# Performance work log

Hardware: AMD Instinct MI355X
Metric: run time of the kernel (lower is better)

The kernel has to match this reference:

```python
import jax, jax.numpy as jnp
import numpy as np


def setup_inputs() -> dict:
    key = jax.random.key(0)
    k1, k2, k3 = jax.random.split(key, 3)
    n_way, n_shot, d, n_query = 5, 10, 1024, 16384
    n_support = n_way * n_shot
    train_imgs = jax.random.normal(k1, (n_support, d), dtype=jnp.float32)
    # one-hot labels: exactly n_shot examples per class (interleaved)
    cls = jnp.tile(jnp.arange(n_way), n_shot)  # [n_support]
    train_labels = jax.nn.one_hot(cls, n_way, dtype=jnp.int64)
    query_imgs = jax.random.normal(k2, (n_query, d), dtype=jnp.float32)
    query_labels = jax.random.randint(k3, (n_query,), 0, n_way)
    return {"train_imgs": train_imgs, "train_labels": train_labels,
            "query_imgs": query_imgs, "query_labels": query_labels}


def reference(train_imgs, train_labels, query_imgs, query_labels):
    # backbone = identity: imgs are already feature embeddings
    n_support, n_way = train_labels.shape
    n_shot = n_support // n_way  # static
    support = train_imgs                      # [n_support, d]
    query = query_imgs                        # [n_query, d]

    # group support features by class: [n_way, n_shot, d]
    cls = jnp.argmax(train_labels, axis=1)
    order = jnp.argsort(cls, stable=True)
    grouped = support[order].reshape(n_way, n_shot, -1)
    mats = jnp.swapaxes(grouped, 1, 2)        # [n_way, d, n_shot]

    # batched reduced SVD (torch.svd some=True -> full_matrices=False)
    U, _, _ = jnp.linalg.svd(mats, full_matrices=False)  # [n_way, d, n_shot]
    Uk = U[:, :, : n_shot - 1]                # [n_way, d, k]

    # projection of queries onto each class subspace: P = Uk Uk^T q
    coeff = jnp.einsum('wdk,qd->wkq', Uk, query)   # [n_way, k, n_query]
    proj = jnp.einsum('wdk,wkq->wqd', Uk, coeff)   # [n_way, n_query, d]
    dist = jnp.sum((query[None, :, :] - proj) ** 2, axis=-1)  # [n_way, n_query]

    logits = -dist.T                           # [n_query, n_way]
    # normalize=False in this configuration
    return jax.nn.log_softmax(logits, axis=1)
```

## Files before the change

### kernel.cpp

```cpp
#include <hip/hip_runtime.h>
#include <stdint.h>


typedef __attribute__((ext_vector_type(4))) float f32x4;
typedef __attribute__((ext_vector_type(8))) short s16x8;

#define WS_G_OFF    0
#define WS_GH_OFF   4096
#define WS_P_OFF    8192
#define WS_Z_OFF    262144

__device__ __forceinline__ unsigned short f2bf(float f) {
  unsigned int u = __float_as_uint(f);
  u += 0x7FFFu + ((u >> 16) & 1u);
  return (unsigned short)(u >> 16);
}

__device__ __forceinline__ bool labels_int64(const int* L) {
  int cnt = 0; bool oddz = true;
  #pragma unroll
  for (int t = 0; t < 20; ++t) {
    int v = L[t];
    if (t & 1) { if (v) oddz = false; }
    else       { if (v) cnt++; }
  }
  return oddz && (cnt == 2);
}

__device__ __forceinline__ int cls_of(const int* L, bool is64, int i) {
  int best = -0x7fffffff, c = 0;
  #pragma unroll
  for (int j = 0; j < 5; ++j) {
    int v = is64 ? L[i * 10 + 2 * j] : L[i * 5 + j];
    if (v > best) { best = v; c = j; }
  }
  return c;
}

__global__ __launch_bounds__(256) void dsn_prep(const float* __restrict__ support,
                                                const int* __restrict__ labels,
                                                double* __restrict__ G,
                                                unsigned short* __restrict__ P) {
  int b = blockIdx.x;
  bool is64 = labels_int64(labels);

  if (b < 69) {
    int wid  = b * 4 + (threadIdx.x >> 6);
    int lane = threadIdx.x & 63;
    if (wid >= 275) return;
    int w = wid / 55, p = wid % 55;
    int a = 0;
    while (p >= 10 - a) { p -= 10 - a; a++; }
    int bb = a + p;

    int myc = (lane < 50) ? cls_of(labels, is64, lane) : -1;
    unsigned long long mask = __ballot(lane < 50 && myc == w);

    unsigned long long m = mask;
    for (int i = 0; i < a; ++i) m &= m - 1;
    int ia = __ffsll((unsigned long long)m) - 1;
    m = mask;
    for (int i = 0; i < bb; ++i) m &= m - 1;
    int ib = __ffsll((unsigned long long)m) - 1;

    const float* A = support + ia * 1024;
    const float* B = support + ib * 1024;
    double acc = 0.0;
    #pragma unroll
    for (int i = 0; i < 16; ++i) {
      int d = lane + 64 * i;
      acc += (double)A[d] * (double)B[d];
    }
    #pragma unroll
    for (int off = 32; off > 0; off >>= 1) acc += __shfl_xor(acc, off);
    if (lane == 0) {
      G[(w * 10 + a) * 10 + bb] = acc;
      G[(w * 10 + bb) * 10 + a] = acc;
    }
  } else {
    int r = b - 69;
    int w = r >> 4, kk = r & 15;
    int t = threadIdx.x;
    unsigned short* Prow = P + r * 1024;
    if (kk >= 10) {
      #pragma unroll
      for (int j = 0; j < 4; ++j) Prow[t + 256 * j] = 0;
      return;
    }
    __shared__ int sid;
    if (t < 64) {
      int myc = (t < 50) ? cls_of(labels, is64, t) : -1;
      unsigned long long mask = __ballot(t < 50 && myc == w);
      if (t == 0) {
        unsigned long long m = mask;
        for (int z = 0; z < kk; ++z) m &= m - 1;
        sid = __ffsll(m) - 1;
      }
    }
    __syncthreads();
    const float* src = support + (size_t)sid * 1024;
    #pragma unroll
    for (int j = 0; j < 4; ++j) Prow[t + 256 * j] = f2bf(src[t + 256 * j]);
  }
}

__global__ __launch_bounds__(64) void dsn_zs(const float* __restrict__ query,
                                             const unsigned short* __restrict__ P,
                                             const double* __restrict__ G,
                                             float* __restrict__ Ghat,
                                             float* __restrict__ Z) {
  if (blockIdx.x < 5) {
    __shared__ float Gf[100], B[100];
    __shared__ float rowk[10], colk[10], vbuf[10], gvbuf[10];
    __shared__ float sbuf;
    __shared__ int   jmx;

    int w = blockIdx.x, t = threadIdx.x;
    bool act = (t < 50);
    int e0 = 2 * t, e1 = 2 * t + 1;
    int i0 = e0 / 10, j0 = e0 % 10;
    int i1 = e1 / 10, j1 = e1 % 10;
    if (!act) { e0 = 0; e1 = 1; i0 = 0; j0 = 0; i1 = 0; j1 = 1; }

    float a0 = 0.f, a1 = 0.f;
    if (act) {
      a0 = (float)G[w * 100 + e0];
      a1 = (float)G[w * 100 + e1];
      Gf[e0] = a0; Gf[e1] = a1;
    }
    __syncthreads();

    #pragma unroll 1
    for (int k = 0; k < 10; ++k) {
      if (act) {
        if (i0 == k) rowk[j0] = a0;
        if (i1 == k) rowk[j1] = a1;
        if (j0 == k) colk[i0] = a0;
        if (j1 == k) colk[i1] = a1;
      }
      __syncthreads();
      float dinv = 1.f / rowk[k];
      float r0 = rowk[j0], c0 = colk[i0];
      float r1 = rowk[j1], c1 = colk[i1];
      __syncthreads();
      if (act) {
        bool ik = (i0 == k), jk = (j0 == k);
        if (ik && jk)        a0 = -dinv;
        else if (ik || jk)   a0 = a0 * dinv;
        else                 a0 -= c0 * r0 * dinv;
        ik = (i1 == k); jk = (j1 == k);
        if (ik && jk)        a1 = -dinv;
        else if (ik || jk)   a1 = a1 * dinv;
        else                 a1 -= c1 * r1 * dinv;
      }
    }
    float ginv0 = -a0, ginv1 = -a1;

    if (act) { B[e0] = ginv0; B[e1] = ginv1; }
    __syncthreads();
    if (t == 0) {
      float m = B[0];
      #pragma unroll
      for (int k = 1; k < 10; ++k) m = fmaxf(m, B[k * 10 + k]);
      sbuf = 1.f / m;
    }
    __syncthreads();
    float rm0 = sbuf;
    if (act) { B[e0] = ginv0 * rm0; B[e1] = ginv1 * rm0; }
    __syncthreads();

    #pragma unroll 1
    for (int sq = 0; sq < 7; ++sq) {
      float s0 = 0.f, s1 = 0.f;
      if (act) {
        #pragma unroll
        for (int k = 0; k < 10; ++k) {
          s0 += B[i0 * 10 + k] * B[k * 10 + j0];
          s1 += B[i1 * 10 + k] * B[k * 10 + j1];
        }
      }
      __syncthreads();
      if (act) { B[e0] = s0; B[e1] = s1; }
      __syncthreads();
      if (t == 0) {
        float m = B[0];
        #pragma unroll
        for (int k = 1; k < 10; ++k) m = fmaxf(m, B[k * 10 + k]);
        sbuf = 1.f / m;
      }
      __syncthreads();
      float rm = sbuf;
      if (act) { B[e0] = s0 * rm; B[e1] = s1 * rm; }
      __syncthreads();
    }

    if (t == 0) {
      int best = 0; float bv = B[0];
      #pragma unroll
      for (int k = 1; k < 10; ++k) {
        float dk = B[k * 10 + k];
        if (dk > bv) { bv = dk; best = k; }
      }
      jmx = best;
    }
    __syncthreads();
    if (t < 10) vbuf[t] = B[t * 10 + jmx];
    __syncthreads();
    #pragma unroll 1
    for (int rf = 0; rf < 2; ++rf) {
      float nv = 0.f;
      if (t < 10) {
        #pragma unroll
        for (int k = 0; k < 10; ++k) nv += B[t * 10 + k] * vbuf[k];
      }
      __syncthreads();
      if (t < 10) vbuf[t] = nv;
      __syncthreads();
    }

    if (t < 10) {
      float gv = 0.f;
      #pragma unroll
      for (int k = 0; k < 10; ++k) gv += Gf[t * 10 + k] * vbuf[k];
      gvbuf[t] = gv;
    }
    __syncthreads();
    if (t == 0) {
      float denom = 0.f;
      #pragma unroll
      for (int k = 0; k < 10; ++k) denom += vbuf[k] * gvbuf[k];
      sbuf = 1.f / denom;
    }
    __syncthreads();
    float rden = sbuf;
    if (act) {
      Ghat[w * 100 + e0] = ginv0 - vbuf[i0] * vbuf[j0] * rden;
      Ghat[w * 100 + e1] = ginv1 - vbuf[i1] * vbuf[j1] * rden;
    }
    return;
  }

  int wid  = blockIdx.x - 5;
  int lane = threadIdx.x;
  int q0   = wid * 16;
  int qrow = lane & 15;
  int kbase = (lane >> 4) * 8;

  const float* qp = query + (size_t)(q0 + qrow) * 1024 + kbase;
  const unsigned short* up = P + qrow * 1024 + kbase;

  f32x4 acc[5];
  #pragma unroll
  for (int w = 0; w < 5; ++w) acc[w] = (f32x4){0.f, 0.f, 0.f, 0.f};

  #pragma unroll 4
  for (int kt = 0; kt < 32; ++kt) {
    const float* qk = qp + kt * 32;
    f32x4 lo = *(const f32x4*)qk;
    f32x4 hi = *(const f32x4*)(qk + 4);
    s16x8 bf;
    bf[0] = (short)f2bf(lo[0]); bf[1] = (short)f2bf(lo[1]);
    bf[2] = (short)f2bf(lo[2]); bf[3] = (short)f2bf(lo[3]);
    bf[4] = (short)f2bf(hi[0]); bf[5] = (short)f2bf(hi[1]);
    bf[6] = (short)f2bf(hi[2]); bf[7] = (short)f2bf(hi[3]);
    const unsigned short* uk = up + kt * 32;
    #pragma unroll
    for (int w = 0; w < 5; ++w) {
      s16x8 av = *(const s16x8*)(uk + w * 16384);
      acc[w] = __builtin_amdgcn_mfma_f32_16x16x32_bf16(av, bf, acc[w], 0, 0, 0);
    }
  }

  int rowbase = (lane >> 4) * 4;
  #pragma unroll
  for (int w = 0; w < 5; ++w) {
    #pragma unroll
    for (int r = 0; r < 4; ++r)
      Z[(size_t)(w * 16 + rowbase + r) * 16384 + q0 + qrow] = acc[w][r];
  }
}

__global__ __launch_bounds__(256) void dsn_post(const float* __restrict__ Ghat,
                                                const float* __restrict__ Z,
                                                float* __restrict__ out) {
  __shared__ float Gh[500];
  int t = threadIdx.x;
  for (int i = t; i < 500; i += 256) Gh[i] = Ghat[i];
  __syncthreads();
  int q = blockIdx.x * 256 + t;

  float zv[50];
  #pragma unroll
  for (int w = 0; w < 5; ++w)
    #pragma unroll
    for (int s = 0; s < 10; ++s)
      zv[w * 10 + s] = Z[(size_t)(w * 16 + s) * 16384 + q];

  float sv[5];
  #pragma unroll
  for (int w = 0; w < 5; ++w) {
    float s = 0.f;
    #pragma unroll
    for (int i = 0; i < 10; ++i) {
      float gz = 0.f;
      #pragma unroll
      for (int j = 0; j < 10; ++j) gz += Gh[w * 100 + i * 10 + j] * zv[w * 10 + j];
      s += zv[w * 10 + i] * gz;
    }
    sv[w] = s;
  }
  float mx = fmaxf(fmaxf(fmaxf(sv[0], sv[1]), fmaxf(sv[2], sv[3])), sv[4]);
  float sum = 0.f;
  #pragma unroll
  for (int w = 0; w < 5; ++w) sum += expf(sv[w] - mx);
  float lse = mx + logf(sum);
  float* o = out + (size_t)q * 5;
  #pragma unroll
  for (int w = 0; w < 5; ++w) o[w] = sv[w] - lse;
}

extern "C" void kernel_launch(void* const* d_in, const int* in_sizes, int n_in,
                              void* d_out, int out_size, void* d_ws, size_t ws_size,
                              hipStream_t stream) {
  const float* support = (const float*)d_in[0];
  const int*   labels  = (const int*)d_in[1];
  const float* query   = (const float*)d_in[2];
  float* out = (float*)d_out;
  char* ws = (char*)d_ws;

  double*         G    = (double*)(ws + WS_G_OFF);
  float*          Ghat = (float*)(ws + WS_GH_OFF);
  unsigned short* P    = (unsigned short*)(ws + WS_P_OFF);
  float*          Z    = (float*)(ws + WS_Z_OFF);

  int nq = in_sizes[2] / 1024;
  int zs_blocks = nq / 16 + 5;
  int post_blocks = nq / 256;

  hipLaunchKernelGGL(dsn_prep, dim3(149), dim3(256), 0, stream, support, labels, G, P);
  hipLaunchKernelGGL(dsn_zs,   dim3(zs_blocks), dim3(64), 0, stream,
                     query, P, G, Ghat, Z);
  hipLaunchKernelGGL(dsn_post, dim3(post_blocks), dim3(256), 0, stream, Ghat, Z, out);
}
```

Before: 43.26 us.

## Rewrite 10x10 Gram inversion with wave-level readlane and pack four waves per block

The small per-class 10x10 inversion, power iteration and rank-one correction now run inside a single wavefront. Each lane holds one matrix row in registers and reads other rows through readlane, replacing shared memory and many __syncthreads barriers. The query projection part now packs four 64-lane waves into each 256-thread block, which cuts the block count by four. The cost is higher register pressure from fully unrolled loops, and the 5 solver blocks each leave three waves idle.

Result: no change. 43.02 us (-0.6%).

```diff
diff --git a/kernel.cpp b/kernel.cpp
--- a/kernel.cpp
+++ b/kernel.cpp
@@ -9,6 +9,8 @@
 #define WS_GH_OFF   4096
 #define WS_P_OFF    8192
 #define WS_Z_OFF    262144
+
+#define RDL(x, l) __uint_as_float(__builtin_amdgcn_readlane(__float_as_uint(x), (l)))
 
 __device__ __forceinline__ unsigned short f2bf(float f) {
   unsigned int u = __float_as_uint(f);
@@ -104,144 +106,115 @@
   }
 }
 
-__global__ __launch_bounds__(64) void dsn_zs(const float* __restrict__ query,
-                                             const unsigned short* __restrict__ P,
-                                             const double* __restrict__ G,
-                                             float* __restrict__ Ghat,
-                                             float* __restrict__ Z) {
+__global__ __launch_bounds__(256) void dsn_zs(const float* __restrict__ query,
+                                              const unsigned short* __restrict__ P,
+                                              const double* __restrict__ G,
+                                              float* __restrict__ Ghat,
+                                              float* __restrict__ Z) {
   if (blockIdx.x < 5) {
-    __shared__ float Gf[100], B[100];
-    __shared__ float rowk[10], colk[10], vbuf[10], gvbuf[10];
-    __shared__ float sbuf;
-    __shared__ int   jmx;
-
-    int w = blockIdx.x, t = threadIdx.x;
-    bool act = (t < 50);
-    int e0 = 2 * t, e1 = 2 * t + 1;
-    int i0 = e0 / 10, j0 = e0 % 10;
-    int i1 = e1 / 10, j1 = e1 % 10;
-    if (!act) { e0 = 0; e1 = 1; i0 = 0; j0 = 0; i1 = 0; j1 = 1; }
-
-    float a0 = 0.f, a1 = 0.f;
-    if (act) {
-      a0 = (float)G[w * 100 + e0];
-      a1 = (float)G[w * 100 + e1];
-      Gf[e0] = a0; Gf[e1] = a1;
-    }
-    __syncthreads();
-
-    #pragma unroll 1
+    if (threadIdx.x >= 64) return;
+    int w = blockIdx.x;
+    int li = threadIdx.x;
+    int rr = (li < 10) ? li : 0;
+    const double* Gr = G + w * 100 + rr * 10;
+
+    float o[10], g[10], h[10];
+    #pragma unroll
+    for (int j = 0; j < 10; ++j) {
+      o[j] = (float)Gr[j];
+      g[j] = o[j];
+      h[j] = (li == j) ? 1.f : 0.f;
+    }
+
+    #pragma unroll
     for (int k = 0; k < 10; ++k) {
-      if (act) {
-        if (i0 == k) rowk[j0] = a0;
-        if (i1 == k) rowk[j1] = a1;
-        if (j0 == k) colk[i0] = a0;
-        if (j1 == k) colk[i1] = a1;
+      float piv = 1.f / RDL(g[k], k);
+      float pg[10], ph[10];
+      #pragma unroll
+      for (int j = 0; j < 10; ++j) {
+        pg[j] = RDL(g[j], k) * piv;
+        ph[j] = RDL(h[j], k) * piv;
       }
-      __syncthreads();
-      float dinv = 1.f / rowk[k];
-      float r0 = rowk[j0], c0 = colk[i0];
-      float r1 = rowk[j1], c1 = colk[i1];
-      __syncthreads();
-      if (act) {
-        bool ik = (i0 == k), jk = (j0 == k);
-        if (ik && jk)        a0 = -dinv;
-        else if (ik || jk)   a0 = a0 * dinv;
-        else                 a0 -= c0 * r0 * dinv;
-        ik = (i1 == k); jk = (j1 == k);
-        if (ik && jk)        a1 = -dinv;
-        else if (ik || jk)   a1 = a1 * dinv;
-        else                 a1 -= c1 * r1 * dinv;
+      float f = g[k];
+      bool isk = (li == k);
+      #pragma unroll
+      for (int j = 0; j < 10; ++j) {
+        g[j] = isk ? pg[j] : g[j] - f * pg[j];
+        h[j] = isk ? ph[j] : h[j] - f * ph[j];
       }
     }
-    float ginv0 = -a0, ginv1 = -a1;
-
-    if (act) { B[e0] = ginv0; B[e1] = ginv1; }
-    __syncthreads();
-    if (t == 0) {
-      float m = B[0];
-      #pragma unroll
-      for (int k = 1; k < 10; ++k) m = fmaxf(m, B[k * 10 + k]);
-      sbuf = 1.f / m;
-    }
-    __syncthreads();
-    float rm0 = sbuf;
-    if (act) { B[e0] = ginv0 * rm0; B[e1] = ginv1 * rm0; }
-    __syncthreads();
-
-    #pragma unroll 1
+
+    float b[10];
+    float d = h[0];
+    #pragma unroll
+    for (int k = 1; k < 10; ++k) d = (li == k) ? h[k] : d;
+    float dm = RDL(d, 0);
+    #pragma unroll
+    for (int k = 1; k < 10; ++k) dm = fmaxf(dm, RDL(d, k));
+    float rn = 1.f / dm;
+    #pragma unroll
+    for (int j = 0; j < 10; ++j) b[j] = h[j] * rn;
+
+    #pragma unroll
     for (int sq = 0; sq < 7; ++sq) {
-      float s0 = 0.f, s1 = 0.f;
-      if (act) {
+      float c[10];
+      #pragma unroll
+      for (int j = 0; j < 10; ++j) {
+        float s = 0.f;
         #pragma unroll
-        for (int k = 0; k < 10; ++k) {
-          s0 += B[i0 * 10 + k] * B[k * 10 + j0];
-          s1 += B[i1 * 10 + k] * B[k * 10 + j1];
-        }
+        for (int k = 0; k < 10; ++k) s += b[k] * RDL(b[j], k);
+        c[j] = s;
       }
-      __syncthreads();
-      if (act) { B[e0] = s0; B[e1] = s1; }
-      __syncthreads();
-      if (t == 0) {
-        float m = B[0];
-        #pragma unroll
-        for (int k = 1; k < 10; ++k) m = fmaxf(m, B[k * 10 + k]);
-        sbuf = 1.f / m;
-      }
-      __syncthreads();
-      float rm = sbuf;
-      if (act) { B[e0] = s0 * rm; B[e1] = s1 * rm; }
-      __syncthreads();
-    }
-
-    if (t == 0) {
-      int best = 0; float bv = B[0];
-      #pragma unroll
-      for (int k = 1; k < 10; ++k) {
-        float dk = B[k * 10 + k];
-        if (dk > bv) { bv = dk; best = k; }
-      }
-      jmx = best;
-    }
-    __syncthreads();
-    if (t < 10) vbuf[t] = B[t * 10 + jmx];
-    __syncthreads();
-    #pragma unroll 1
+      float dd = c[0];
+      #pragma unroll
+      for (int k = 1; k < 10; ++k) dd = (li == k) ? c[k] : dd;
+      float m = RDL(dd, 0);
+      #pragma unroll
+      for (int k = 1; k < 10; ++k) m = fmaxf(m, RDL(dd, k));
+      float rm = 1.f / m;
+      #pragma unroll
+      for (int j = 0; j < 10; ++j) b[j] = c[j] * rm;
+    }
+
+    float db = b[0];
+    #pragma unroll
+    for (int k = 1; k < 10; ++k) db = (li == k) ? b[k] : db;
+    int jmx = 0;
+    float bv = RDL(db, 0);
+    #pragma unroll
+    for (int k = 1; k < 10; ++k) {
+      float t2 = RDL(db, k);
+      if (t2 > bv) { bv = t2; jmx = k; }
+    }
+    float v = b[0];
+    #pragma unroll
+    for (int k = 1; k < 10; ++k) v = (jmx == k) ? b[k] : v;
+    #pragma unroll
     for (int rf = 0; rf < 2; ++rf) {
       float nv = 0.f;
-      if (t < 10) {
-        #pragma unroll
-        for (int k = 0; k < 10; ++k) nv += B[t * 10 + k] * vbuf[k];
-      }
-      __syncthreads();
-      if (t < 10) vbuf[t] = nv;
-      __syncthreads();
-    }
-
-    if (t < 10) {
-      float gv = 0.f;
-      #pragma unroll
-      for (int k = 0; k < 10; ++k) gv += Gf[t * 10 + k] * vbuf[k];
-      gvbuf[t] = gv;
-    }
-    __syncthreads();
-    if (t == 0) {
-      float denom = 0.f;
-      #pragma unroll
-      for (int k = 0; k < 10; ++k) denom += vbuf[k] * gvbuf[k];
-      sbuf = 1.f / denom;
-    }
-    __syncthreads();
-    float rden = sbuf;
-    if (act) {
-      Ghat[w * 100 + e0] = ginv0 - vbuf[i0] * vbuf[j0] * rden;
-      Ghat[w * 100 + e1] = ginv1 - vbuf[i1] * vbuf[j1] * rden;
+      #pragma unroll
+      for (int k = 0; k < 10; ++k) nv += b[k] * RDL(v, k);
+      v = nv;
+    }
+
+    float gv = 0.f;
+    #pragma unroll
+    for (int k = 0; k < 10; ++k) gv += o[k] * RDL(v, k);
+    float tn = v * gv;
+    float denom = RDL(tn, 0);
+    #pragma unroll
+    for (int k = 1; k < 10; ++k) denom += RDL(tn, k);
+    float rden = 1.f / denom;
+    if (li < 10) {
+      #pragma unroll
+      for (int j = 0; j < 10; ++j)
+        Ghat[w * 100 + li * 10 + j] = h[j] - v * RDL(v, j) * rden;
     }
     return;
   }
 
-  int wid  = blockIdx.x - 5;
-  int lane = threadIdx.x;
+  int wid  = (blockIdx.x - 5) * 4 + (threadIdx.x >> 6);
+  int lane = threadIdx.x & 63;
   int q0   = wid * 16;
   int qrow = lane & 15;
   int kbase = (lane >> 4) * 8;
@@ -334,11 +307,11 @@
   float*          Z    = (float*)(ws + WS_Z_OFF);
 
   int nq = in_sizes[2] / 1024;
-  int zs_blocks = nq / 16 + 5;
+  int zs_blocks = nq / 64 + 5;
   int post_blocks = nq / 256;
 
   hipLaunchKernelGGL(dsn_prep, dim3(149), dim3(256), 0, stream, support, labels, G, P);
-  hipLaunchKernelGGL(dsn_zs,   dim3(zs_blocks), dim3(64), 0, stream,
+  hipLaunchKernelGGL(dsn_zs,   dim3(zs_blocks), dim3(256), 0, stream,
                      query, P, G, Ghat, Z);
   hipLaunchKernelGGL(dsn_post, dim3(post_blocks), dim3(256), 0, stream, Ghat, Z, out);
 }
```
